# Kernel tuning notes

Measured on AMD Instinct MI355X. Metric: run time of the kernel, lower is better.

Reference implementation:

```python
import jax, jax.numpy as jnp
import numpy as np
from functools import partial

ALPHA = 2.0  # surrogate sharpness

@partial(jax.custom_vjp, nondiff_argnums=(1,))
def spike(x, alpha):
    # Heaviside forward, atan surrogate backward
    return (x >= 0.0).astype(x.dtype)

def _spike_fwd(x, alpha):
    return spike(x, alpha), x

def _spike_bwd(alpha, x, g):
    grad = (alpha / 2.0) / (1.0 + (jnp.pi / 2.0 * alpha * x) ** 2)
    return (g * grad,)

spike.defvjp(_spike_fwd, _spike_bwd)


def setup_inputs() -> dict:
    key = jax.random.key(0)
    k1, k2, k3 = jax.random.split(key, 3)
    B, T, H = 128, 2048, 512
    TAU_INIT, TH_INIT = 8.0, 0.5
    x_seq = jax.random.normal(k1, (B, T, 2), dtype=jnp.float32)
    W_in = jax.random.normal(k2, (2, H), dtype=jnp.float32) * (1.0 / np.sqrt(2.0))
    b_in = jnp.zeros((H,), dtype=jnp.float32)
    # PLIF: sigmoid(w_tau) = 1/tau  =>  w_tau = -log(tau - 1)
    w_tau = jnp.full((H,), -np.log(TAU_INIT - 1.0), dtype=jnp.float32)
    threshold = jnp.full((H,), TH_INIT, dtype=jnp.float32)
    W_out = jax.random.normal(k3, (H, 2), dtype=jnp.float32) * (1.0 / np.sqrt(H))
    b_out = jnp.zeros((2,), dtype=jnp.float32)
    return {"x_seq": x_seq, "W_in": W_in, "b_in": b_in,
            "w_tau": w_tau, "threshold": threshold,
            "W_out": W_out, "b_out": b_out}


def reference(x_seq, W_in, b_in, w_tau, threshold, W_out, b_out):
    B, T, _ = x_seq.shape
    H = W_in.shape[1]
    cur = x_seq @ W_in + b_in                      # [B, T, H]
    decay = jax.nn.sigmoid(w_tau)                  # [H], = 1/tau

    def step(v, c):
        v = v + (c - v) * decay                    # leaky integration
        s = spike(v - threshold, ALPHA)            # threshold + surrogate
        v = v * (1.0 - s)                          # hard reset
        return v, s

    v0 = jnp.zeros((B, H), dtype=x_seq.dtype)
    _, s_seq = jax.lax.scan(step, v0, jnp.transpose(cur, (1, 0, 2)))  # s_seq: [T, B, H]
    rate = s_seq.mean(axis=0)                      # [B, H]
    return rate @ W_out + b_out                    # [B, 2]
```

## Files before the change

### kernel.cpp

```cpp
#include <hip/hip_runtime.h>
#include <math.h>

#define NB 128
#define NT 2048
#define NH 512
#define HBLK 64
#define HCHUNKS (NH / HBLK)
#define NCH 4
#define WARM 256
#define MAIN (NT / NCH)

#define STEP2_BODY(q, COUNT)                                      \
    do {                                                          \
        float cdA = fmaf((q).x, A0, fmaf((q).y, A1, Bd));         \
        float vnA = fmaf(vp, K, cdA);                             \
        vp = sp ? cdA : vnA;                                      \
        sp = (vp >= th);                                          \
        if (COUNT) cnt += sp ? 1 : 0;                             \
        float cdB = fmaf((q).z, A0, fmaf((q).w, A1, Bd));         \
        float vnB = fmaf(vp, K, cdB);                             \
        vp = sp ? cdB : vnB;                                      \
        sp = (vp >= th);                                          \
        if (COUNT) cnt += sp ? 1 : 0;                             \
    } while (0)

__global__ __launch_bounds__(HBLK, 4)
void snn_scan_kernel(const float* __restrict__ x,
                     const float* __restrict__ W_in,
                     const float* __restrict__ b_in,
                     const float* __restrict__ w_tau,
                     const float* __restrict__ thr_p,
                     const float* __restrict__ W_out,
                     const float* __restrict__ b_out,
                     float* __restrict__ out) {
    __shared__ float4 xs[(WARM + MAIN) / 2];

    const int blk = blockIdx.x;
    const int c   = blk & (NCH - 1);
    const int hc  = (blk >> 2) & (HCHUNKS - 1);
    const int b   = blk >> 5;
    const int h   = hc * HBLK + threadIdx.x;

    const int warm = c ? WARM : 0;
    const int g4   = (c * MAIN - warm) >> 1;
    const int n4   = (warm + MAIN) >> 1;

    const float4* __restrict__ xb =
        (const float4*)(x + (size_t)b * (NT * 2)) + g4;
    for (int i = threadIdx.x; i < n4; i += HBLK)
        xs[i] = xb[i];

    const float w0 = W_in[h];
    const float w1 = W_in[NH + h];
    const float bi = b_in[h];
    const float wt = w_tau[h];
    const float decay = (wt >= 0.0f)
        ? (1.0f / (1.0f + expf(-wt)))
        : ({ float e = expf(wt); e / (1.0f + e); });
    const float th = thr_p[h];

    const float A0 = w0 * decay;
    const float A1 = w1 * decay;
    const float Bd = bi * decay;
    const float K  = 1.0f - decay;

    __syncthreads();

    float vp = 0.0f;
    bool  sp = false;
    int   cnt = 0;

    if (c) {
        #pragma unroll 8
        for (int i = 0; i < WARM / 2; ++i) {
            float4 q = xs[i];
            STEP2_BODY(q, 0);
        }
    }

    const int w4 = c ? (WARM / 2) : 0;
    #pragma unroll 8
    for (int i = 0; i < MAIN / 2; ++i) {
        float4 q = xs[w4 + i];
        STEP2_BODY(q, 1);
    }

    float rate = (float)cnt * (1.0f / (float)NT);
    float o0 = rate * W_out[2 * h];
    float o1 = rate * W_out[2 * h + 1];

    #pragma unroll
    for (int off = 32; off > 0; off >>= 1) {
        o0 += __shfl_down(o0, off, 64);
        o1 += __shfl_down(o1, off, 64);
    }
    if (threadIdx.x == 0) {
        if (hc == 0 && c == 0) {
            o0 += b_out[0];
            o1 += b_out[1];
        }
        atomicAdd(&out[b * 2 + 0], o0);
        atomicAdd(&out[b * 2 + 1], o1);
    }
}

extern "C" void kernel_launch(void* const* d_in, const int* in_sizes, int n_in,
                              void* d_out, int out_size, void* d_ws, size_t ws_size,
                              hipStream_t stream) {
    const float* x     = (const float*)d_in[0];
    const float* W_in  = (const float*)d_in[1];
    const float* b_in  = (const float*)d_in[2];
    const float* w_tau = (const float*)d_in[3];
    const float* thr   = (const float*)d_in[4];
    const float* W_out = (const float*)d_in[5];
    const float* b_out = (const float*)d_in[6];
    float* out = (float*)d_out;

    hipMemsetAsync(out, 0, (size_t)out_size * sizeof(float), stream);
    hipLaunchKernelGGL(snn_scan_kernel,
                       dim3(NB * HCHUNKS * NCH), dim3(HBLK), 0, stream,
                       x, W_in, b_in, w_tau, thr, W_out, b_out, out);
}
```

Before: 99.90 us.

## Interleave two time chunks per thread with register double-buffered global loads

Each block now handles two of the four time chunks per thread, interleaving two independent recurrences so one hides the latency of the other. The shared-memory staging of x is replaced by direct, software-prefetched global float4 loads, with an asm zero offset to keep the loads from being hoisted or merged. The warm-up length is halved, which cuts redundant recomputation but relies on the state converging faster. The grid is halved and launch bounds lowered, trading block-level parallelism and occupancy for per-thread instruction-level parallelism.

```diff
diff --git a/kernel.cpp b/kernel.cpp
--- a/kernel.cpp
+++ b/kernel.cpp
@@ -5,26 +5,38 @@
 #define NT 2048
 #define NH 512
 #define HBLK 64
-#define HCHUNKS (NH / HBLK)
+#define HCHUNKS (NH / NB * 16)
+#undef HCHUNKS
+#define HCHUNKS 8
 #define NCH 4
-#define WARM 256
+#define WARM 128
 #define MAIN (NT / NCH)
+#define WB (WARM / 8)
+#define MB (MAIN / 8)
 
-#define STEP2_BODY(q, COUNT)                                      \
+#define STEP2(qx, qy, qz, qw, vp, sp, cnt, CNT)                   \
     do {                                                          \
-        float cdA = fmaf((q).x, A0, fmaf((q).y, A1, Bd));         \
-        float vnA = fmaf(vp, K, cdA);                             \
-        vp = sp ? cdA : vnA;                                      \
+        float cd1 = fmaf((qx), A0, fmaf((qy), A1, Bd));           \
+        float vn1 = fmaf(vp, K, cd1);                             \
+        vp = sp ? cd1 : vn1;                                      \
         sp = (vp >= th);                                          \
-        if (COUNT) cnt += sp ? 1 : 0;                             \
-        float cdB = fmaf((q).z, A0, fmaf((q).w, A1, Bd));         \
-        float vnB = fmaf(vp, K, cdB);                             \
-        vp = sp ? cdB : vnB;                                      \
+        if (CNT) cnt += sp ? 1 : 0;                               \
+        float cd2 = fmaf((qz), A0, fmaf((qw), A1, Bd));           \
+        float vn2 = fmaf(vp, K, cd2);                             \
+        vp = sp ? cd2 : vn2;                                      \
         sp = (vp >= th);                                          \
-        if (COUNT) cnt += sp ? 1 : 0;                             \
+        if (CNT) cnt += sp ? 1 : 0;                               \
     } while (0)
 
-__global__ __launch_bounds__(HBLK, 4)
+#define PROC8(q0, q1, q2, q3, vp, sp, cnt, CNT)                   \
+    do {                                                          \
+        STEP2(q0.x, q0.y, q0.z, q0.w, vp, sp, cnt, CNT);          \
+        STEP2(q1.x, q1.y, q1.z, q1.w, vp, sp, cnt, CNT);          \
+        STEP2(q2.x, q2.y, q2.z, q2.w, vp, sp, cnt, CNT);          \
+        STEP2(q3.x, q3.y, q3.z, q3.w, vp, sp, cnt, CNT);          \
+    } while (0)
+
+__global__ __launch_bounds__(HBLK, 2)
 void snn_scan_kernel(const float* __restrict__ x,
                      const float* __restrict__ W_in,
                      const float* __restrict__ b_in,
@@ -33,22 +45,13 @@
                      const float* __restrict__ W_out,
                      const float* __restrict__ b_out,
                      float* __restrict__ out) {
-    __shared__ float4 xs[(WARM + MAIN) / 2];
-
     const int blk = blockIdx.x;
-    const int c   = blk & (NCH - 1);
-    const int hc  = (blk >> 2) & (HCHUNKS - 1);
-    const int b   = blk >> 5;
+    const int p   = blk & 1;
+    const int hc  = (blk >> 1) & (HCHUNKS - 1);
+    const int b   = blk >> 4;
     const int h   = hc * HBLK + threadIdx.x;
-
-    const int warm = c ? WARM : 0;
-    const int g4   = (c * MAIN - warm) >> 1;
-    const int n4   = (warm + MAIN) >> 1;
-
-    const float4* __restrict__ xb =
-        (const float4*)(x + (size_t)b * (NT * 2)) + g4;
-    for (int i = threadIdx.x; i < n4; i += HBLK)
-        xs[i] = xb[i];
+    const int cA  = 2 * p;
+    const int cB  = 2 * p + 1;
 
     const float w0 = W_in[h];
     const float w1 = W_in[NH + h];
@@ -64,28 +67,57 @@
     const float Bd = bi * decay;
     const float K  = 1.0f - decay;
 
-    __syncthreads();
+    int vz;
+    asm volatile("v_mov_b32 %0, 0" : "=v"(vz));
 
-    float vp = 0.0f;
-    bool  sp = false;
-    int   cnt = 0;
+    const float4* row = (const float4*)(x + (size_t)b * (NT * 2));
+    const float4* mA  = row + cA * (MAIN / 2);
+    const float4* mB  = row + cB * (MAIN / 2);
+    const float4* wA  = cA ? (mA - WARM / 2) : row;
+    const float4* wB  = mB - WARM / 2;
 
-    if (c) {
-        #pragma unroll 8
-        for (int i = 0; i < WARM / 2; ++i) {
-            float4 q = xs[i];
-            STEP2_BODY(q, 0);
-        }
+#define LD(ptr, idx) (ptr)[(idx) + vz]
+
+    float vpA = 0.0f, vpB = 0.0f;
+    bool  spA = false, spB = false;
+    int   cntA = 0,  cntB = 0;
+
+    float4 ca0 = LD(wA, 0), ca1 = LD(wA, 1), ca2 = LD(wA, 2), ca3 = LD(wA, 3);
+    float4 cb0 = LD(wB, 0), cb1 = LD(wB, 1), cb2 = LD(wB, 2), cb3 = LD(wB, 3);
+
+    #pragma unroll 2
+    for (int i = 0; i < WB; ++i) {
+        const float4* nA = (i < WB - 1) ? (wA + 4 * (i + 1)) : mA;
+        const float4* nB = (i < WB - 1) ? (wB + 4 * (i + 1)) : mB;
+        float4 na0 = LD(nA, 0), na1 = LD(nA, 1), na2 = LD(nA, 2), na3 = LD(nA, 3);
+        float4 nb0 = LD(nB, 0), nb1 = LD(nB, 1), nb2 = LD(nB, 2), nb3 = LD(nB, 3);
+
+        PROC8(ca0, ca1, ca2, ca3, vpA, spA, cntA, 0);
+        PROC8(cb0, cb1, cb2, cb3, vpB, spB, cntB, 0);
+
+        ca0 = na0; ca1 = na1; ca2 = na2; ca3 = na3;
+        cb0 = nb0; cb1 = nb1; cb2 = nb2; cb3 = nb3;
     }
 
-    const int w4 = c ? (WARM / 2) : 0;
-    #pragma unroll 8
-    for (int i = 0; i < MAIN / 2; ++i) {
-        float4 q = xs[w4 + i];
-        STEP2_BODY(q, 1);
+    if (p == 0) { vpA = 0.0f; spA = false; }
+
+    #pragma unroll 2
+    for (int j = 0; j < MB; ++j) {
+        const int nx = ((j + 1) & (MB - 1)) * 4;
+        float4 na0 = LD(mA, nx + 0), na1 = LD(mA, nx + 1),
+               na2 = LD(mA, nx + 2), na3 = LD(mA, nx + 3);
+        float4 nb0 = LD(mB, nx + 0), nb1 = LD(mB, nx + 1),
+               nb2 = LD(mB, nx + 2), nb3 = LD(mB, nx + 3);
+
+        PROC8(ca0, ca1, ca2, ca3, vpA, spA, cntA, 1);
+        PROC8(cb0, cb1, cb2, cb3, vpB, spB, cntB, 1);
+
+        ca0 = na0; ca1 = na1; ca2 = na2; ca3 = na3;
+        cb0 = nb0; cb1 = nb1; cb2 = nb2; cb3 = nb3;
     }
+#undef LD
 
-    float rate = (float)cnt * (1.0f / (float)NT);
+    float rate = (float)(cntA + cntB) * (1.0f / (float)NT);
     float o0 = rate * W_out[2 * h];
     float o1 = rate * W_out[2 * h + 1];
 
@@ -95,7 +127,7 @@
         o1 += __shfl_down(o1, off, 64);
     }
     if (threadIdx.x == 0) {
-        if (hc == 0 && c == 0) {
+        if (hc == 0 && p == 0) {
             o0 += b_out[0];
             o1 += b_out[1];
         }
@@ -118,6 +150,6 @@
 
     hipMemsetAsync(out, 0, (size_t)out_size * sizeof(float), stream);
     hipLaunchKernelGGL(snn_scan_kernel,
-                       dim3(NB * HCHUNKS * NCH), dim3(HBLK), 0, stream,
+                       dim3(NB * HCHUNKS * 2), dim3(HBLK), 0, stream,
                        x, W_in, b_in, w_tau, thr, W_out, b_out, out);
 }
```

Measured after the change: 114.4 us. 1.15x slower.

## Stream inputs from global memory with register prefetch and shorten warmup

Applied to the files above, without the earlier changes.

Removes the shared-memory staging of the input sequence and its barrier. Each thread instead loads float4 chunks directly from global memory with a two-deep register prefetch pipeline, using an opaque zero offset to keep the loads as vector loads. The warmup length for the chunked time split is also halved, which reduces redundant recurrence steps. The risks are global load latency stalling the serial recurrence, and slightly more approximation error from the shorter warmup.

```diff
diff --git a/kernel.cpp b/kernel.cpp
--- a/kernel.cpp
+++ b/kernel.cpp
@@ -5,23 +5,31 @@
 #define NT 2048
 #define NH 512
 #define HBLK 64
-#define HCHUNKS (NH / HBLK)
+#define HCHUNKS 8
 #define NCH 4
-#define WARM 256
+#define WARM 128
 #define MAIN (NT / NCH)
+#define WB (WARM / 8)
+#define MB (MAIN / 8)
 
-#define STEP2_BODY(q, COUNT)                                      \
+#define STEP2(q, CNT)                                             \
     do {                                                          \
-        float cdA = fmaf((q).x, A0, fmaf((q).y, A1, Bd));         \
-        float vnA = fmaf(vp, K, cdA);                             \
-        vp = sp ? cdA : vnA;                                      \
+        float cd1 = fmaf((q).x, A0, fmaf((q).y, A1, Bd));         \
+        float vn1 = fmaf(vp, K, cd1);                             \
+        vp = sp ? cd1 : vn1;                                      \
         sp = (vp >= th);                                          \
-        if (COUNT) cnt += sp ? 1 : 0;                             \
-        float cdB = fmaf((q).z, A0, fmaf((q).w, A1, Bd));         \
-        float vnB = fmaf(vp, K, cdB);                             \
-        vp = sp ? cdB : vnB;                                      \
+        if (CNT) cnt += sp ? 1 : 0;                               \
+        float cd2 = fmaf((q).z, A0, fmaf((q).w, A1, Bd));         \
+        float vn2 = fmaf(vp, K, cd2);                             \
+        vp = sp ? cd2 : vn2;                                      \
         sp = (vp >= th);                                          \
-        if (COUNT) cnt += sp ? 1 : 0;                             \
+        if (CNT) cnt += sp ? 1 : 0;                               \
+    } while (0)
+
+#define PROC8(q0, q1, q2, q3, CNT)                                \
+    do {                                                          \
+        STEP2(q0, CNT); STEP2(q1, CNT);                           \
+        STEP2(q2, CNT); STEP2(q3, CNT);                           \
     } while (0)
 
 __global__ __launch_bounds__(HBLK, 4)
@@ -33,22 +41,11 @@
                      const float* __restrict__ W_out,
                      const float* __restrict__ b_out,
                      float* __restrict__ out) {
-    __shared__ float4 xs[(WARM + MAIN) / 2];
-
     const int blk = blockIdx.x;
     const int c   = blk & (NCH - 1);
     const int hc  = (blk >> 2) & (HCHUNKS - 1);
     const int b   = blk >> 5;
     const int h   = hc * HBLK + threadIdx.x;
-
-    const int warm = c ? WARM : 0;
-    const int g4   = (c * MAIN - warm) >> 1;
-    const int n4   = (warm + MAIN) >> 1;
-
-    const float4* __restrict__ xb =
-        (const float4*)(x + (size_t)b * (NT * 2)) + g4;
-    for (int i = threadIdx.x; i < n4; i += HBLK)
-        xs[i] = xb[i];
 
     const float w0 = W_in[h];
     const float w1 = W_in[NH + h];
@@ -64,26 +61,45 @@
     const float Bd = bi * decay;
     const float K  = 1.0f - decay;
 
-    __syncthreads();
+    int vz;
+    asm volatile("v_mov_b32 %0, 0" : "=v"(vz));
+
+    const int warm = c ? WARM : 0;
+    const int wb   = c ? WB : 0;
+    const int nb   = wb + MB;
+    const int start_t = c * MAIN - warm;
+    const float4* __restrict__ base =
+        (const float4*)(x + (size_t)b * (NT * 2)) + (start_t >> 1);
+
+#define LD(idx) base[(idx) + vz]
 
     float vp = 0.0f;
     bool  sp = false;
     int   cnt = 0;
 
-    if (c) {
-        #pragma unroll 8
-        for (int i = 0; i < WARM / 2; ++i) {
-            float4 q = xs[i];
-            STEP2_BODY(q, 0);
-        }
+    float4 a0 = LD(0), a1 = LD(1), a2 = LD(2), a3 = LD(3);
+    float4 b0 = LD(4), b1 = LD(5), b2 = LD(6), b3 = LD(7);
+
+    int i = 0;
+    #pragma unroll 2
+    for (; i < wb; ++i) {
+        const int nx = (i + 2) * 4;
+        float4 n0 = LD(nx), n1 = LD(nx + 1), n2 = LD(nx + 2), n3 = LD(nx + 3);
+        PROC8(a0, a1, a2, a3, 0);
+        a0 = b0; a1 = b1; a2 = b2; a3 = b3;
+        b0 = n0; b1 = n1; b2 = n2; b3 = n3;
     }
-
-    const int w4 = c ? (WARM / 2) : 0;
-    #pragma unroll 8
-    for (int i = 0; i < MAIN / 2; ++i) {
-        float4 q = xs[w4 + i];
-        STEP2_BODY(q, 1);
+    #pragma unroll 2
+    for (; i < nb - 2; ++i) {
+        const int nx = (i + 2) * 4;
+        float4 n0 = LD(nx), n1 = LD(nx + 1), n2 = LD(nx + 2), n3 = LD(nx + 3);
+        PROC8(a0, a1, a2, a3, 1);
+        a0 = b0; a1 = b1; a2 = b2; a3 = b3;
+        b0 = n0; b1 = n1; b2 = n2; b3 = n3;
     }
+    PROC8(a0, a1, a2, a3, 1);
+    PROC8(b0, b1, b2, b3, 1);
+#undef LD
 
     float rate = (float)cnt * (1.0f / (float)NT);
     float o0 = rate * W_out[2 * h];
```

Measured after the change: 119.5 us. +19.7%, slower.
